# Kernel tuning notes

Hardware: AMD Instinct MI355X
Metric: run time of the kernel (lower is better)

## Reference

```python
import jax, jax.numpy as jnp
import numpy as np

N_NODES = 100000
N_EDGES = 600000
DIM = 128  # 2 * size_in


def gcn_layer(x, W, b, src, dst, n):
    # GCNConv (PyG, normalize=True, add_self_loops=True):
    # h = x @ W; norm = deg^-1/2[src] * deg^-1/2[dst] with self-loops; out = scatter_add + b
    h = x @ W
    loops = jnp.arange(n)
    s = jnp.concatenate([src, loops])
    d = jnp.concatenate([dst, loops])
    deg = jax.ops.segment_sum(jnp.ones_like(s, dtype=x.dtype), d, num_segments=n)
    dinv = jnp.where(deg > 0, deg ** -0.5, 0.0).astype(x.dtype)
    norm = dinv[s] * dinv[d]  # [E+N]
    msg = h[s] * norm[:, None]  # [E+N, DIM] -- dominant gather traffic
    out = jax.ops.segment_sum(msg, d, num_segments=n)
    return out + b


def setup_inputs() -> dict:
    key = jax.random.key(0)
    k = jax.random.split(key, 6)
    x = jax.random.normal(k[0], (N_NODES, DIM), dtype=jnp.float32)
    W1 = jax.random.normal(k[1], (DIM, DIM), dtype=jnp.float32) * (DIM ** -0.5)
    b1 = jax.random.normal(k[2], (DIM,), dtype=jnp.float32) * 0.02
    W2 = jax.random.normal(k[3], (DIM, DIM), dtype=jnp.float32) * (DIM ** -0.5)
    b2 = jax.random.normal(k[4], (DIM,), dtype=jnp.float32) * 0.02
    edge_index = jax.random.randint(k[5], (2, N_EDGES), 0, N_NODES, dtype=jnp.int64 if jax.config.jax_enable_x64 else jnp.int32)
    return {"x": x, "W1": W1, "b1": b1, "W2": W2, "b2": b2, "edge_index": edge_index}


def reference(x, W1, b1, W2, b2, edge_index):
    src, dst = edge_index[0], edge_index[1]
    out = gcn_layer(x, W1, b1, src, dst, N_NODES)
    out = jnp.tanh(out)
    out = gcn_layer(out, W2, b2, src, dst, N_NODES)
    return out
```

## Files before the change

kernel.cpp:

```cpp
#include <hip/hip_runtime.h>
#include <math.h>

#define NBLK 256

typedef __attribute__((ext_vector_type(8))) short short8v;
typedef __attribute__((ext_vector_type(4))) float f32x4;

__device__ __forceinline__ unsigned cvt_pk_bf16(float lo, float hi) {
    unsigned r;
    asm("v_cvt_pk_bf16_f32 %0, %1, %2" : "=v"(r) : "v"(lo), "v"(hi));
    return r;
}
__device__ __forceinline__ float bf_lo(unsigned u) { return __uint_as_float(u << 16); }
__device__ __forceinline__ float bf_hi(unsigned u) { return __uint_as_float(u & 0xffff0000u); }

__device__ __forceinline__ float fast_tanh(float x) {
    float cx = fminf(fmaxf(x, -15.f), 15.f);
    float e = __expf(2.f * cx);
    return (e - 1.f) / (e + 1.f);
}


__global__ __launch_bounds__(NBLK) void zero_k(int* p, int n) {
    int i = blockIdx.x * blockDim.x + threadIdx.x;
    if (i < n) p[i] = 0;
}

__global__ __launch_bounds__(NBLK) void count_k(const int* __restrict__ dst, int E, int* __restrict__ cnt) {
    int e = blockIdx.x * blockDim.x + threadIdx.x;
    if (e < E) atomicAdd(&cnt[dst[e]], 1);
}

__global__ __launch_bounds__(NBLK) void scan1_k(const int* __restrict__ cnt, int n,
                                                int* __restrict__ off, int* __restrict__ bsum) {
    __shared__ int ls[NBLK];
    int base = blockIdx.x * 1024 + threadIdx.x * 4;
    int v[4]; int s = 0;
#pragma unroll
    for (int i = 0; i < 4; ++i) {
        int idx = base + i;
        v[i] = (idx < n) ? cnt[idx] : 0;
        s += v[i];
    }
    ls[threadIdx.x] = s;
    __syncthreads();
    for (int o = 1; o < NBLK; o <<= 1) {
        int t = (threadIdx.x >= (unsigned)o) ? ls[threadIdx.x - o] : 0;
        __syncthreads();
        ls[threadIdx.x] += t;
        __syncthreads();
    }
    int run = ls[threadIdx.x] - s;
#pragma unroll
    for (int i = 0; i < 4; ++i) {
        int idx = base + i;
        if (idx < n) off[idx] = run;
        run += v[i];
    }
    if (threadIdx.x == NBLK - 1) bsum[blockIdx.x] = ls[NBLK - 1];
}

__global__ void scan2_k(int* bsum, int nb) {
    __shared__ int ls[128];
    int t = threadIdx.x;
    int v = (t < nb) ? bsum[t] : 0;
    ls[t] = v;
    __syncthreads();
    for (int o = 1; o < 128; o <<= 1) {
        int tv = (t >= o) ? ls[t - o] : 0;
        __syncthreads();
        ls[t] += tv;
        __syncthreads();
    }
    if (t < nb) bsum[t] = ls[t] - v;
}

__global__ __launch_bounds__(NBLK) void scan3_k(int* __restrict__ off, const int* __restrict__ bsum,
                                                const int* __restrict__ cnt, float* __restrict__ dinv, int n) {
    int i = blockIdx.x * blockDim.x + threadIdx.x;
    if (i < n) {
        off[i] += bsum[i >> 10];
        dinv[i] = rsqrtf((float)(cnt[i] + 1));
    }
}

__global__ __launch_bounds__(NBLK) void fill_k(const int* __restrict__ src, const int* __restrict__ dst, int E,
                                               const int* __restrict__ off, int* __restrict__ cursor,
                                               const float* __restrict__ dinv,
                                               int* __restrict__ srcs, float* __restrict__ norms) {
    int e = blockIdx.x * blockDim.x + threadIdx.x;
    if (e >= E) return;
    int s = src[e], d = dst[e];
    int pos = atomicAdd(&cursor[d], 1);
    int idx = off[d] + pos;
    srcs[idx] = s;
    norms[idx] = dinv[s] * dinv[d];
}

__global__ __launch_bounds__(NBLK) void wcast_k(const float* __restrict__ W1, const float* __restrict__ W2,
                                                ushort* __restrict__ Wt1, ushort* __restrict__ Wt2) {
    int i = blockIdx.x * blockDim.x + threadIdx.x;
    int which = i >> 14;
    int idx = i & 16383;
    const float* W = which ? W2 : W1;
    ushort* Wt = which ? Wt2 : Wt1;
    int k = idx >> 7, c = idx & 127;
    float v = W[idx];
    Wt[c * 128 + k] = (ushort)(cvt_pk_bf16(v, v) & 0xffffu);
}


template<int CVT>
__global__ __launch_bounds__(NBLK, 2) void gemm_mfma_k(const void* __restrict__ Xin,
                                                       const ushort* __restrict__ Wt,
                                                       ushort* __restrict__ Hb, int nrows, int nbt) {
    __shared__ unsigned Xls[64 * 64];
    const int t = threadIdx.x;
    const int lane = t & 63;
    const int wv = t >> 6;
    const int l15 = lane & 15;
    const int g = lane >> 4;

    short8v B[4][8];
#pragma unroll
    for (int ks = 0; ks < 4; ++ks)
#pragma unroll
        for (int nt = 0; nt < 8; ++nt) {
            int col = nt * 16 + l15;
            int k0 = ks * 32 + g * 8;
            B[ks][nt] = *(const short8v*)&Wt[col * 128 + k0];
        }

    for (int bt = blockIdx.x; bt < nbt; bt += gridDim.x) {
        int row0 = bt * 64;
        __syncthreads();
        {
            int r = t >> 2;
            int rg = row0 + r;
#pragma unroll
            for (int j = 0; j < 4; ++j) {
                int u = (t & 3) + 4 * j;
                uint4 val;
                if (CVT) {
                    float4 f0 = make_float4(0.f,0.f,0.f,0.f), f1 = f0;
                    if (rg < nrows) {
                        const float4* Xv = (const float4*)Xin;
                        f0 = Xv[(size_t)rg * 32 + u * 2];
                        f1 = Xv[(size_t)rg * 32 + u * 2 + 1];
                    }
                    val.x = cvt_pk_bf16(f0.x, f0.y); val.y = cvt_pk_bf16(f0.z, f0.w);
                    val.z = cvt_pk_bf16(f1.x, f1.y); val.w = cvt_pk_bf16(f1.z, f1.w);
                } else {
                    val = make_uint4(0u,0u,0u,0u);
                    if (rg < nrows) val = ((const uint4*)Xin)[(size_t)rg * 16 + u];
                }
                *(uint4*)&Xls[r * 64 + ((u ^ (r & 15)) << 2)] = val;
            }
        }
        __syncthreads();

        short8v A[4];
#pragma unroll
        for (int ks = 0; ks < 4; ++ks) {
            int r = wv * 16 + l15;
            int u = ks * 4 + g;
            A[ks] = *(short8v*)&Xls[r * 64 + ((u ^ l15) << 2)];
        }

        f32x4 acc[8];
#pragma unroll
        for (int nt = 0; nt < 8; ++nt) acc[nt] = (f32x4){0.f, 0.f, 0.f, 0.f};
#pragma unroll
        for (int ks = 0; ks < 4; ++ks)
#pragma unroll
            for (int nt = 0; nt < 8; ++nt)
                acc[nt] = __builtin_amdgcn_mfma_f32_16x16x32_bf16(A[ks], B[ks][nt], acc[nt], 0, 0, 0);

        int trow0 = row0 + wv * 16;
#pragma unroll
        for (int nt = 0; nt < 8; ++nt)
#pragma unroll
            for (int q = 0; q < 4; ++q) {
                int row = trow0 + g * 4 + q;
                if (row < nrows)
                    Hb[(size_t)row * 128 + nt * 16 + l15] =
                        (ushort)(cvt_pk_bf16(acc[nt][q], acc[nt][q]) & 0xffffu);
            }
    }
}


#define UPK_FMA(u4, nm, A) { \
    A[0] = fmaf(bf_lo((u4).x), (nm), A[0]); A[1] = fmaf(bf_hi((u4).x), (nm), A[1]); \
    A[2] = fmaf(bf_lo((u4).y), (nm), A[2]); A[3] = fmaf(bf_hi((u4).y), (nm), A[3]); \
    A[4] = fmaf(bf_lo((u4).z), (nm), A[4]); A[5] = fmaf(bf_hi((u4).z), (nm), A[5]); \
    A[6] = fmaf(bf_lo((u4).w), (nm), A[6]); A[7] = fmaf(bf_hi((u4).w), (nm), A[7]); }

template<int OUT_BF16>
__global__ __launch_bounds__(NBLK) void aggregate_k(const ushort* __restrict__ Hb,
                                                    const int* __restrict__ off, const int* __restrict__ cnt,
                                                    const int* __restrict__ srcs, const float* __restrict__ norms,
                                                    const float* __restrict__ dinv, const float* __restrict__ bias,
                                                    void* __restrict__ outp, int n, int apply_tanh) {
    int node = (blockIdx.x * blockDim.x + threadIdx.x) >> 3;
    if (node >= n) return;
    int il = threadIdx.x & 7;

    const uint4* Hv = (const uint4*)Hb;
    float acc[16];
#pragma unroll
    for (int i = 0; i < 16; ++i) acc[i] = 0.f;

    float dv = dinv[node];
    float w = dv * dv;
    {
        size_t rb = (size_t)node * 16;
        uint4 s0 = Hv[rb + il], s1 = Hv[rb + 8 + il];
        UPK_FMA(s0, w, acc);
        UPK_FMA(s1, w, (acc + 8));
    }

    int e0 = off[node];
    int deg = cnt[node];
    int eLast = e0 + deg - 1;
    for (int b = 0; b < deg; b += 4) {
        int sidx[4]; float nm[4];
#pragma unroll
        for (int q = 0; q < 4; ++q) {
            bool v = (b + q) < deg;
            int ce = v ? (e0 + b + q) : eLast;
            sidx[q] = srcs[ce];
            nm[q] = v ? norms[ce] : 0.f;
        }
        uint4 g0[4], g1[4];
#pragma unroll
        for (int q = 0; q < 4; ++q) {
            size_t r = (size_t)sidx[q] * 16;
            g0[q] = Hv[r + il];
            g1[q] = Hv[r + 8 + il];
        }
#pragma unroll
        for (int q = 0; q < 4; ++q) {
            UPK_FMA(g0[q], nm[q], acc);
            UPK_FMA(g1[q], nm[q], (acc + 8));
        }
    }

    float4 b0 = *(const float4*)&bias[il * 8];
    float4 b1 = *(const float4*)&bias[il * 8 + 4];
    float4 b2 = *(const float4*)&bias[64 + il * 8];
    float4 b3 = *(const float4*)&bias[64 + il * 8 + 4];
    acc[0] += b0.x; acc[1] += b0.y; acc[2]  += b0.z; acc[3]  += b0.w;
    acc[4] += b1.x; acc[5] += b1.y; acc[6]  += b1.z; acc[7]  += b1.w;
    acc[8] += b2.x; acc[9] += b2.y; acc[10] += b2.z; acc[11] += b2.w;
    acc[12] += b3.x; acc[13] += b3.y; acc[14] += b3.z; acc[15] += b3.w;

    if (apply_tanh) {
#pragma unroll
        for (int i = 0; i < 16; ++i) acc[i] = fast_tanh(acc[i]);
    }

    if (OUT_BF16) {
        uint4 o0, o1;
        o0.x = cvt_pk_bf16(acc[0],  acc[1]);  o0.y = cvt_pk_bf16(acc[2],  acc[3]);
        o0.z = cvt_pk_bf16(acc[4],  acc[5]);  o0.w = cvt_pk_bf16(acc[6],  acc[7]);
        o1.x = cvt_pk_bf16(acc[8],  acc[9]);  o1.y = cvt_pk_bf16(acc[10], acc[11]);
        o1.z = cvt_pk_bf16(acc[12], acc[13]); o1.w = cvt_pk_bf16(acc[14], acc[15]);
        uint4* O = (uint4*)outp;
        O[(size_t)node * 16 + il] = o0;
        O[(size_t)node * 16 + 8 + il] = o1;
    } else {
        float* O = (float*)outp;
        *(float4*)&O[(size_t)node * 128 + il * 8]      = make_float4(acc[0], acc[1], acc[2], acc[3]);
        *(float4*)&O[(size_t)node * 128 + il * 8 + 4]  = make_float4(acc[4], acc[5], acc[6], acc[7]);
        *(float4*)&O[(size_t)node * 128 + 64 + il * 8]     = make_float4(acc[8], acc[9], acc[10], acc[11]);
        *(float4*)&O[(size_t)node * 128 + 64 + il * 8 + 4] = make_float4(acc[12], acc[13], acc[14], acc[15]);
    }
}


extern "C" void kernel_launch(void* const* d_in, const int* in_sizes, int n_in,
                              void* d_out, int out_size, void* d_ws, size_t ws_size,
                              hipStream_t stream) {
    const float* x  = (const float*)d_in[0];
    const float* W1 = (const float*)d_in[1];
    const float* b1 = (const float*)d_in[2];
    const float* W2 = (const float*)d_in[3];
    const float* b2 = (const float*)d_in[4];
    const int*   ei = (const int*)d_in[5];

    const int N = in_sizes[0] / 128;
    const int E = in_sizes[5] / 2;
    const int* src = ei;
    const int* dst = ei + E;

    char* p = (char*)d_ws;
    ushort* hb    = (ushort*)p; p += (size_t)N * 128 * sizeof(ushort);
    ushort* tb    = (ushort*)p; p += (size_t)N * 128 * sizeof(ushort);
    int*    cnt   = (int*)p;    p += (size_t)N * sizeof(int);
    int*    cursor= (int*)p;    p += (size_t)N * sizeof(int);
    int*    off   = (int*)p;    p += (size_t)N * sizeof(int);
    float*  dinv  = (float*)p;  p += (size_t)N * sizeof(float);
    int*    srcs  = (int*)p;    p += (size_t)E * sizeof(int);
    float*  norms = (float*)p;  p += (size_t)E * sizeof(float);
    ushort* Wt1   = (ushort*)p; p += 16384 * sizeof(ushort);
    ushort* Wt2   = (ushort*)p; p += 16384 * sizeof(ushort);
    int*    bsum  = (int*)p;    p += 1024;

    const int nb = (N + 1023) / 1024;
    const int nbt = (N + 63) / 64;

    zero_k <<<(2 * N + NBLK - 1) / NBLK, NBLK, 0, stream>>>(cnt, 2 * N);
    count_k<<<(E + NBLK - 1) / NBLK, NBLK, 0, stream>>>(dst, E, cnt);
    scan1_k<<<nb, NBLK, 0, stream>>>(cnt, N, off, bsum);
    scan2_k<<<1, 128, 0, stream>>>(bsum, nb);
    scan3_k<<<(N + NBLK - 1) / NBLK, NBLK, 0, stream>>>(off, bsum, cnt, dinv, N);
    fill_k <<<(E + NBLK - 1) / NBLK, NBLK, 0, stream>>>(src, dst, E, off, cursor, dinv, srcs, norms);
    wcast_k<<<128, NBLK, 0, stream>>>(W1, W2, Wt1, Wt2);

    const int agg_blocks = (N * 8 + NBLK - 1) / NBLK;

    gemm_mfma_k<1><<<512, NBLK, 0, stream>>>(x, Wt1, hb, N, nbt);
    aggregate_k<1><<<agg_blocks, NBLK, 0, stream>>>(hb, off, cnt, srcs, norms, dinv, b1, tb, N, 1);
    gemm_mfma_k<0><<<512, NBLK, 0, stream>>>(tb, Wt2, hb, N, nbt);
    aggregate_k<0><<<agg_blocks, NBLK, 0, stream>>>(hb, off, cnt, srcs, norms, dinv, b2, d_out, N, 0);
}
```

Before: 183.8 us.

## Fold symmetric degree normalization into GEMM epilogue and drop per-edge norms array

Rows of the GEMM output are pre-scaled by dinv[src], and the aggregation sum is scaled by dinv[dst] at the end, so the per-edge norms array is no longer needed. The fill kernel now writes only source indices, using a cursor initialised to the offsets in scan3, which removes the off and dinv gathers and the norm write. The aggregation loop loses one per-edge load, and the zeroing kernel clears half as much memory. In exchange, rounding now happens on the dinv-scaled bf16 values, which may shift numerics slightly.

```diff
diff --git a/kernel.cpp b/kernel.cpp
--- a/kernel.cpp
+++ b/kernel.cpp
@@ -76,25 +76,23 @@
 }
 
 __global__ __launch_bounds__(NBLK) void scan3_k(int* __restrict__ off, const int* __restrict__ bsum,
-                                                const int* __restrict__ cnt, float* __restrict__ dinv, int n) {
+                                                const int* __restrict__ cnt, int* __restrict__ cursor,
+                                                float* __restrict__ dinv, int n) {
     int i = blockIdx.x * blockDim.x + threadIdx.x;
     if (i < n) {
-        off[i] += bsum[i >> 10];
+        int o = off[i] + bsum[i >> 10];
+        off[i] = o;
+        cursor[i] = o;
         dinv[i] = rsqrtf((float)(cnt[i] + 1));
     }
 }
 
 __global__ __launch_bounds__(NBLK) void fill_k(const int* __restrict__ src, const int* __restrict__ dst, int E,
-                                               const int* __restrict__ off, int* __restrict__ cursor,
-                                               const float* __restrict__ dinv,
-                                               int* __restrict__ srcs, float* __restrict__ norms) {
+                                               int* __restrict__ cursor, int* __restrict__ srcs) {
     int e = blockIdx.x * blockDim.x + threadIdx.x;
     if (e >= E) return;
-    int s = src[e], d = dst[e];
-    int pos = atomicAdd(&cursor[d], 1);
-    int idx = off[d] + pos;
-    srcs[idx] = s;
-    norms[idx] = dinv[s] * dinv[d];
+    int idx = atomicAdd(&cursor[dst[e]], 1);
+    srcs[idx] = src[e];
 }
 
 __global__ __launch_bounds__(NBLK) void wcast_k(const float* __restrict__ W1, const float* __restrict__ W2,
@@ -113,7 +111,8 @@
 template<int CVT>
 __global__ __launch_bounds__(NBLK, 2) void gemm_mfma_k(const void* __restrict__ Xin,
                                                        const ushort* __restrict__ Wt,
-                                                       ushort* __restrict__ Hb, int nrows, int nbt) {
+                                                       const float* __restrict__ dinv,
+                                                       ushort* __restrict__ Gb, int nrows, int nbt) {
     __shared__ unsigned Xls[64 * 64];
     const int t = threadIdx.x;
     const int lane = t & 63;
@@ -177,14 +176,22 @@
                 acc[nt] = __builtin_amdgcn_mfma_f32_16x16x32_bf16(A[ks], B[ks][nt], acc[nt], 0, 0, 0);
 
         int trow0 = row0 + wv * 16;
+        float dv[4];
+#pragma unroll
+        for (int q = 0; q < 4; ++q) {
+            int row = trow0 + g * 4 + q;
+            dv[q] = (row < nrows) ? dinv[row] : 0.f;
+        }
 #pragma unroll
         for (int nt = 0; nt < 8; ++nt)
 #pragma unroll
             for (int q = 0; q < 4; ++q) {
                 int row = trow0 + g * 4 + q;
-                if (row < nrows)
-                    Hb[(size_t)row * 128 + nt * 16 + l15] =
-                        (ushort)(cvt_pk_bf16(acc[nt][q], acc[nt][q]) & 0xffffu);
+                if (row < nrows) {
+                    float val = acc[nt][q] * dv[q];
+                    Gb[(size_t)row * 128 + nt * 16 + l15] =
+                        (ushort)(cvt_pk_bf16(val, val) & 0xffffu);
+                }
             }
     }
 }
@@ -197,47 +204,41 @@
     A[6] = fmaf(bf_lo((u4).w), (nm), A[6]); A[7] = fmaf(bf_hi((u4).w), (nm), A[7]); }
 
 template<int OUT_BF16>
-__global__ __launch_bounds__(NBLK) void aggregate_k(const ushort* __restrict__ Hb,
+__global__ __launch_bounds__(NBLK) void aggregate_k(const ushort* __restrict__ Gb,
                                                     const int* __restrict__ off, const int* __restrict__ cnt,
-                                                    const int* __restrict__ srcs, const float* __restrict__ norms,
+                                                    const int* __restrict__ srcs,
                                                     const float* __restrict__ dinv, const float* __restrict__ bias,
                                                     void* __restrict__ outp, int n, int apply_tanh) {
     int node = (blockIdx.x * blockDim.x + threadIdx.x) >> 3;
     if (node >= n) return;
     int il = threadIdx.x & 7;
 
-    const uint4* Hv = (const uint4*)Hb;
-    float acc[16];
-#pragma unroll
-    for (int i = 0; i < 16; ++i) acc[i] = 0.f;
-
-    float dv = dinv[node];
-    float w = dv * dv;
-    {
-        size_t rb = (size_t)node * 16;
-        uint4 s0 = Hv[rb + il], s1 = Hv[rb + 8 + il];
-        UPK_FMA(s0, w, acc);
-        UPK_FMA(s1, w, (acc + 8));
-    }
+    const uint4* Gv = (const uint4*)Gb;
+    size_t rb = (size_t)node * 16;
+    uint4 s0 = Gv[rb + il], s1 = Gv[rb + 8 + il];
+    float acc[16] = {
+        bf_lo(s0.x), bf_hi(s0.x), bf_lo(s0.y), bf_hi(s0.y),
+        bf_lo(s0.z), bf_hi(s0.z), bf_lo(s0.w), bf_hi(s0.w),
+        bf_lo(s1.x), bf_hi(s1.x), bf_lo(s1.y), bf_hi(s1.y),
+        bf_lo(s1.z), bf_hi(s1.z), bf_lo(s1.w), bf_hi(s1.w)
+    };
 
     int e0 = off[node];
     int deg = cnt[node];
-    int eLast = e0 + deg - 1;
     for (int b = 0; b < deg; b += 4) {
         int sidx[4]; float nm[4];
 #pragma unroll
         for (int q = 0; q < 4; ++q) {
             bool v = (b + q) < deg;
-            int ce = v ? (e0 + b + q) : eLast;
-            sidx[q] = srcs[ce];
-            nm[q] = v ? norms[ce] : 0.f;
+            sidx[q] = v ? srcs[e0 + b + q] : node;
+            nm[q] = v ? 1.f : 0.f;
         }
         uint4 g0[4], g1[4];
 #pragma unroll
         for (int q = 0; q < 4; ++q) {
             size_t r = (size_t)sidx[q] * 16;
-            g0[q] = Hv[r + il];
-            g1[q] = Hv[r + 8 + il];
+            g0[q] = Gv[r + il];
+            g1[q] = Gv[r + 8 + il];
         }
 #pragma unroll
         for (int q = 0; q < 4; ++q) {
@@ -246,14 +247,19 @@
         }
     }
 
+    float dvn = dinv[node];
     float4 b0 = *(const float4*)&bias[il * 8];
     float4 b1 = *(const float4*)&bias[il * 8 + 4];
     float4 b2 = *(const float4*)&bias[64 + il * 8];
     float4 b3 = *(const float4*)&bias[64 + il * 8 + 4];
-    acc[0] += b0.x; acc[1] += b0.y; acc[2]  += b0.z; acc[3]  += b0.w;
-    acc[4] += b1.x; acc[5] += b1.y; acc[6]  += b1.z; acc[7]  += b1.w;
-    acc[8] += b2.x; acc[9] += b2.y; acc[10] += b2.z; acc[11] += b2.w;
-    acc[12] += b3.x; acc[13] += b3.y; acc[14] += b3.z; acc[15] += b3.w;
+    acc[0]  = fmaf(acc[0],  dvn, b0.x); acc[1]  = fmaf(acc[1],  dvn, b0.y);
+    acc[2]  = fmaf(acc[2],  dvn, b0.z); acc[3]  = fmaf(acc[3],  dvn, b0.w);
+    acc[4]  = fmaf(acc[4],  dvn, b1.x); acc[5]  = fmaf(acc[5],  dvn, b1.y);
+    acc[6]  = fmaf(acc[6],  dvn, b1.z); acc[7]  = fmaf(acc[7],  dvn, b1.w);
+    acc[8]  = fmaf(acc[8],  dvn, b2.x); acc[9]  = fmaf(acc[9],  dvn, b2.y);
+    acc[10] = fmaf(acc[10], dvn, b2.z); acc[11] = fmaf(acc[11], dvn, b2.w);
+    acc[12] = fmaf(acc[12], dvn, b3.x); acc[13] = fmaf(acc[13], dvn, b3.y);
+    acc[14] = fmaf(acc[14], dvn, b3.z); acc[15] = fmaf(acc[15], dvn, b3.w);
 
     if (apply_tanh) {
 #pragma unroll
@@ -271,8 +277,8 @@
         O[(size_t)node * 16 + 8 + il] = o1;
     } else {
         float* O = (float*)outp;
-        *(float4*)&O[(size_t)node * 128 + il * 8]      = make_float4(acc[0], acc[1], acc[2], acc[3]);
-        *(float4*)&O[(size_t)node * 128 + il * 8 + 4]  = make_float4(acc[4], acc[5], acc[6], acc[7]);
+        *(float4*)&O[(size_t)node * 128 + il * 8]          = make_float4(acc[0], acc[1], acc[2], acc[3]);
+        *(float4*)&O[(size_t)node * 128 + il * 8 + 4]      = make_float4(acc[4], acc[5], acc[6], acc[7]);
         *(float4*)&O[(size_t)node * 128 + 64 + il * 8]     = make_float4(acc[8], acc[9], acc[10], acc[11]);
         *(float4*)&O[(size_t)node * 128 + 64 + il * 8 + 4] = make_float4(acc[12], acc[13], acc[14], acc[15]);
     }
@@ -295,14 +301,13 @@
     const int* dst = ei + E;
 
     char* p = (char*)d_ws;
-    ushort* hb    = (ushort*)p; p += (size_t)N * 128 * sizeof(ushort);
+    ushort* gb    = (ushort*)p; p += (size_t)N * 128 * sizeof(ushort);
     ushort* tb    = (ushort*)p; p += (size_t)N * 128 * sizeof(ushort);
     int*    cnt   = (int*)p;    p += (size_t)N * sizeof(int);
     int*    cursor= (int*)p;    p += (size_t)N * sizeof(int);
     int*    off   = (int*)p;    p += (size_t)N * sizeof(int);
     float*  dinv  = (float*)p;  p += (size_t)N * sizeof(float);
     int*    srcs  = (int*)p;    p += (size_t)E * sizeof(int);
-    float*  norms = (float*)p;  p += (size_t)E * sizeof(float);
     ushort* Wt1   = (ushort*)p; p += 16384 * sizeof(ushort);
     ushort* Wt2   = (ushort*)p; p += 16384 * sizeof(ushort);
     int*    bsum  = (int*)p;    p += 1024;
@@ -310,18 +315,18 @@
     const int nb = (N + 1023) / 1024;
     const int nbt = (N + 63) / 64;
 
-    zero_k <<<(2 * N + NBLK - 1) / NBLK, NBLK, 0, stream>>>(cnt, 2 * N);
+    zero_k <<<(N + NBLK - 1) / NBLK, NBLK, 0, stream>>>(cnt, N);
     count_k<<<(E + NBLK - 1) / NBLK, NBLK, 0, stream>>>(dst, E, cnt);
     scan1_k<<<nb, NBLK, 0, stream>>>(cnt, N, off, bsum);
     scan2_k<<<1, 128, 0, stream>>>(bsum, nb);
-    scan3_k<<<(N + NBLK - 1) / NBLK, NBLK, 0, stream>>>(off, bsum, cnt, dinv, N);
-    fill_k <<<(E + NBLK - 1) / NBLK, NBLK, 0, stream>>>(src, dst, E, off, cursor, dinv, srcs, norms);
+    scan3_k<<<(N + NBLK - 1) / NBLK, NBLK, 0, stream>>>(off, bsum, cnt, cursor, dinv, N);
+    fill_k <<<(E + NBLK - 1) / NBLK, NBLK, 0, stream>>>(src, dst, E, cursor, srcs);
     wcast_k<<<128, NBLK, 0, stream>>>(W1, W2, Wt1, Wt2);
 
     const int agg_blocks = (N * 8 + NBLK - 1) / NBLK;
 
-    gemm_mfma_k<1><<<512, NBLK, 0, stream>>>(x, Wt1, hb, N, nbt);
-    aggregate_k<1><<<agg_blocks, NBLK, 0, stream>>>(hb, off, cnt, srcs, norms, dinv, b1, tb, N, 1);
-    gemm_mfma_k<0><<<512, NBLK, 0, stream>>>(tb, Wt2, hb, N, nbt);
-    aggregate_k<0><<<agg_blocks, NBLK, 0, stream>>>(hb, off, cnt, srcs, norms, dinv, b2, d_out, N, 0);
-}
+    gemm_mfma_k<1><<<512, NBLK, 0, stream>>>(x, Wt1, dinv, gb, N, nbt);
+    aggregate_k<1><<<agg_blocks, NBLK, 0, stream>>>(gb, off, cnt, srcs, dinv, b1, tb, N, 1);
+    gemm_mfma_k<0><<<512, NBLK, 0, stream>>>(tb, Wt2, dinv, gb, N, nbt);
+    aggregate_k<0><<<agg_blocks, NBLK, 0, stream>>>(gb, off, cnt, srcs, dinv, b2, d_out, N, 0);
+}
```

New measurement: 207.3 us. 12.8% more time.
